# Optimization experiments

Hardware: AMD Instinct MI355X
Metric: run time of the kernel (lower is better)

The kernel has to match this reference:

```python
import jax, jax.numpy as jnp
import numpy as np

D_MODEL = 1024
NUM_HEADS = 16
LN_EPS = 1e-5


def setup_inputs() -> dict:
    key = jax.random.key(0)
    ks = jax.random.split(key, 7)
    B, S, D = 8, 1024, D_MODEL
    x = jax.random.normal(ks[0], (B, S, D), dtype=jnp.float32)
    # LayerNorm params (torch defaults: weight=1, bias=0; randomize slightly)
    ln_gamma = jnp.ones((D,), jnp.float32) + 0.02 * jax.random.normal(ks[1], (D,), jnp.float32)
    ln_beta = 0.02 * jax.random.normal(ks[2], (D,), jnp.float32)
    # nn.MultiheadAttention params: packed in_proj [3D, D], out_proj [D, D]
    scale = 1.0 / np.sqrt(D)
    in_proj_w = scale * jax.random.normal(ks[3], (3 * D, D), dtype=jnp.float32)
    in_proj_b = jnp.zeros((3 * D,), jnp.float32)
    out_proj_w = scale * jax.random.normal(ks[4], (D, D), dtype=jnp.float32)
    out_proj_b = jnp.zeros((D,), jnp.float32)
    return {
        "x": x,
        "ln_gamma": ln_gamma,
        "ln_beta": ln_beta,
        "in_proj_w": in_proj_w,
        "in_proj_b": in_proj_b,
        "out_proj_w": out_proj_w,
        "out_proj_b": out_proj_b,
    }


def reference(x, ln_gamma, ln_beta, in_proj_w, in_proj_b, out_proj_w, out_proj_b):
    B, S, D = x.shape
    H = NUM_HEADS
    Dh = D // H

    residual = x
    # LayerNorm (torch eps=1e-5)
    mu = jnp.mean(x, axis=-1, keepdims=True)
    var = jnp.mean(jnp.square(x - mu), axis=-1, keepdims=True)
    xn = (x - mu) * jax.lax.rsqrt(var + LN_EPS) * ln_gamma + ln_beta

    # Packed QKV projection: y = xn @ in_proj_w.T + in_proj_b
    qkv = jnp.einsum("bsd,ed->bse", xn, in_proj_w) + in_proj_b  # [B,S,3D]
    q, k, v = jnp.split(qkv, 3, axis=-1)

    def heads(t):  # [B,S,D] -> [B,H,S,Dh]
        return t.reshape(B, S, H, Dh).transpose(0, 2, 1, 3)

    q, k, v = heads(q), heads(k), heads(v)

    scores = jnp.einsum("bhsd,bhtd->bhst", q, k) / np.sqrt(Dh)  # [B,H,S,S]
    probs = jax.nn.softmax(scores, axis=-1)
    ctx = jnp.einsum("bhst,bhtd->bhsd", probs, v)  # [B,H,S,Dh]
    ctx = ctx.transpose(0, 2, 1, 3).reshape(B, S, D)

    attn_out = jnp.einsum("bsd,ed->bse", ctx, out_proj_w) + out_proj_b
    # (need_weights=True would also expose probs.mean over heads; math above
    #  matches the explicit non-flash path torch falls back to)
    return attn_out + residual
```

## Files before the change

### kernel.cpp

```cpp
#include <hip/hip_runtime.h>
#include <hip/hip_bf16.h>

typedef __bf16 bf16;
typedef __bf16 bf16x8 __attribute__((ext_vector_type(8)));
typedef __bf16 bf16x4 __attribute__((ext_vector_type(4)));
typedef float  f32x4  __attribute__((ext_vector_type(4)));

#define D_MODEL 1024
#define S_LEN   1024
#define NHEAD   16
#define DH      64

#define AS1 __attribute__((address_space(1)))
#define AS3 __attribute__((address_space(3)))

__global__ void cvt_kernel(const float* __restrict__ w1, bf16* __restrict__ o1, int n1,
                           const float* __restrict__ w2, bf16* __restrict__ o2, int n2) {
    int i = blockIdx.x * blockDim.x + threadIdx.x;
    const int stride = gridDim.x * blockDim.x;
    for (; i < n1 + n2; i += stride) {
        const float4 v = (i < n1) ? ((const float4*)w1)[i] : ((const float4*)w2)[i - n1];
        bf16x4 r;
        r[0] = (bf16)v.x; r[1] = (bf16)v.y; r[2] = (bf16)v.z; r[3] = (bf16)v.w;
        if (i < n1) ((bf16x4*)o1)[i] = r; else ((bf16x4*)o2)[i - n1] = r;
    }
}

__global__ __launch_bounds__(256) void ln_kernel(const float* __restrict__ x,
        const float* __restrict__ gamma, const float* __restrict__ beta,
        bf16* __restrict__ xn) {
    const int row = blockIdx.x;
    const int tid = threadIdx.x;
    const float4 v = ((const float4*)(x + (size_t)row * D_MODEL))[tid];
    float s  = v.x + v.y + v.z + v.w;
    float s2 = v.x*v.x + v.y*v.y + v.z*v.z + v.w*v.w;
    #pragma unroll
    for (int d = 1; d < 64; d <<= 1) { s += __shfl_xor(s, d); s2 += __shfl_xor(s2, d); }
    __shared__ float red[8];
    const int wave = tid >> 6;
    if ((tid & 63) == 0) { red[wave] = s; red[4 + wave] = s2; }
    __syncthreads();
    s  = red[0] + red[1] + red[2] + red[3];
    s2 = red[4] + red[5] + red[6] + red[7];
    const float mu   = s * (1.0f / D_MODEL);
    const float var  = s2 * (1.0f / D_MODEL) - mu * mu;
    const float rstd = rsqrtf(var + 1e-5f);
    const float4 g = ((const float4*)gamma)[tid];
    const float4 b = ((const float4*)beta)[tid];
    bf16x4 o;
    o[0] = (bf16)((v.x - mu) * rstd * g.x + b.x);
    o[1] = (bf16)((v.y - mu) * rstd * g.y + b.y);
    o[2] = (bf16)((v.z - mu) * rstd * g.z + b.z);
    o[3] = (bf16)((v.w - mu) * rstd * g.w + b.w);
    ((bf16x4*)(xn + (size_t)row * D_MODEL))[tid] = o;
}

#define GEMM_MAIN_LOOP(Ab, Wb, K)                                                        \
    f32x4 acc[4][4] = {};                                                                \
    for (int kt = 0; kt < (K); kt += 64) {                                               \
        _Pragma("unroll")                                                                \
        for (int i = 0; i < 4; ++i) {                                                    \
            const int L = i * 256 + tid;                                                 \
            const int r = L >> 3, blk = L & 7;                                           \
            const int src = (blk ^ (r & 7)) * 8;                                         \
            __builtin_amdgcn_global_load_lds(                                            \
                (const AS1 void*)((Ab) + (size_t)r * (K) + kt + src),                    \
                (AS3 void*)(As + L * 8), 16, 0, 0);                                      \
            __builtin_amdgcn_global_load_lds(                                            \
                (const AS1 void*)((Wb) + (size_t)r * (K) + kt + src),                    \
                (AS3 void*)(Bs + L * 8), 16, 0, 0);                                      \
        }                                                                                \
        __syncthreads();                                                                 \
        _Pragma("unroll")                                                                \
        for (int kk = 0; kk < 2; ++kk) {                                                 \
            bf16x8 af[4], bfm[4];                                                        \
            _Pragma("unroll")                                                            \
            for (int m = 0; m < 4; ++m) {                                                \
                const int R = wr * 64 + m * 16 + (lane & 15);                            \
                af[m] = *(const bf16x8*)(As + R * 64 +                                   \
                            (((kk * 4 + (lane >> 4)) ^ (R & 7)) << 3));                  \
            }                                                                            \
            _Pragma("unroll")                                                            \
            for (int n = 0; n < 4; ++n) {                                                \
                const int R = wc * 64 + n * 16 + (lane & 15);                            \
                bfm[n] = *(const bf16x8*)(Bs + R * 64 +                                  \
                            (((kk * 4 + (lane >> 4)) ^ (R & 7)) << 3));                  \
            }                                                                            \
            _Pragma("unroll")                                                            \
            for (int m = 0; m < 4; ++m)                                                  \
                _Pragma("unroll")                                                        \
                for (int n = 0; n < 4; ++n)                                              \
                    acc[m][n] = __builtin_amdgcn_mfma_f32_16x16x32_bf16(                 \
                        af[m], bfm[n], acc[m][n], 0, 0, 0);                              \
        }                                                                                \
        __syncthreads();                                                                 \
    }

#define XCD_REMAP()                                                                      \
    const int f = blockIdx.y * gridDim.x + blockIdx.x;                                   \
    const int xcd = f & 7;                                                               \
    const int rank = f >> 3;                                                             \
    const int brow = (xcd * 8 + (rank & 7)) * 128;                                       \
    const int bcol = (rank >> 3) * 128;

__global__ __launch_bounds__(256, 4) void gemm_qkv(
        const bf16* __restrict__ A, const bf16* __restrict__ W,
        const float* __restrict__ bias,
        bf16* __restrict__ q, bf16* __restrict__ k, bf16* __restrict__ vt) {
    __shared__ bf16 smem[2 * 128 * 64];
    bf16* As = smem;
    bf16* Bs = smem + 128 * 64;
    const int tid = threadIdx.x;
    const int lane = tid & 63;
    const int wave = tid >> 6;
    const int wr = wave >> 1, wc = wave & 1;
    XCD_REMAP()
    const bf16* Ab = A + (size_t)brow * 1024;
    const bf16* Wb = W + (size_t)bcol * 1024;

    GEMM_MAIN_LOOP(Ab, Wb, 1024)

    const int region = bcol >> 10;
    const int c = lane & 15, hh = lane >> 4;
    if (region == 2) {
        #pragma unroll
        for (int m = 0; m < 4; ++m) {
            #pragma unroll
            for (int n = 0; n < 4; ++n) {
                const int col = bcol + wc * 64 + n * 16 + c;
                const float bb = bias[col];
                const int e = col & 1023;
                const int h = e >> 6, dh = e & 63;
                const int row0 = brow + wr * 64 + m * 16 + hh * 4;
                const int b = row0 >> 10, s0 = row0 & 1023;
                const int bh = b * NHEAD + h;
                bf16x4 pk;
                #pragma unroll
                for (int j = 0; j < 4; ++j) pk[j] = (bf16)(acc[m][n][j] + bb);
                *(bf16x4*)(vt + ((size_t)bh * DH + dh) * S_LEN + s0) = pk;
            }
        }
    } else {
        const float qsc = (region == 0) ? 0.1803368801111244f : 1.0f;
        #pragma unroll
        for (int m = 0; m < 4; ++m) {
            #pragma unroll
            for (int n = 0; n < 4; ++n) {
                const int col = wc * 64 + n * 16 + c;
                const float bb = bias[bcol + col];
                #pragma unroll
                for (int j = 0; j < 4; ++j) {
                    const int row = wr * 64 + m * 16 + hh * 4 + j;
                    const int pb = (col >> 3) ^ (row & 7);
                    smem[row * 128 + pb * 8 + (col & 7)] = (bf16)((acc[m][n][j] + bb) * qsc);
                }
            }
        }
        __syncthreads();
        bf16* dst = (region == 0) ? q : k;
        #pragma unroll
        for (int i = 0; i < 8; ++i) {
            const int idx = i * 256 + tid;
            const int row = idx >> 4;
            const int bb = idx & 15;
            const bf16x8 vv = *(const bf16x8*)(smem + row * 128 + (bb ^ (row & 7)) * 8);
            const int grow = brow + row;
            const int s = grow & 1023, b = grow >> 10;
            const int col0 = bcol + bb * 8;
            const int e = col0 & 1023;
            const int h = e >> 6, dh = e & 63;
            *(bf16x8*)(dst + ((size_t)(b * NHEAD + h) * S_LEN + s) * DH + dh) = vv;
        }
    }
}

__global__ __launch_bounds__(256, 4) void gemm_out(
        const bf16* __restrict__ A, const bf16* __restrict__ W,
        const float* __restrict__ bias, const float* __restrict__ resid,
        float* __restrict__ out) {
    __shared__ bf16 smem[2 * 128 * 64];
    bf16* As = smem;
    bf16* Bs = smem + 128 * 64;
    const int tid = threadIdx.x;
    const int lane = tid & 63;
    const int wave = tid >> 6;
    const int wr = wave >> 1, wc = wave & 1;
    XCD_REMAP()
    const bf16* Ab = A + (size_t)brow * 1024;
    const bf16* Wb = W + (size_t)bcol * 1024;

    GEMM_MAIN_LOOP(Ab, Wb, 1024)

    #pragma unroll
    for (int m = 0; m < 4; ++m) {
        #pragma unroll
        for (int n = 0; n < 4; ++n) {
            const int col = bcol + wc * 64 + n * 16 + (lane & 15);
            const float bb = bias[col];
            #pragma unroll
            for (int j = 0; j < 4; ++j) {
                const int row = brow + wr * 64 + m * 16 + (lane >> 4) * 4 + j;
                const size_t idx = (size_t)row * D_MODEL + col;
                out[idx] = acc[m][n][j] + bb + resid[idx];
            }
        }
    }
}

__global__ __launch_bounds__(256, 3) void attn_kernel(
        const bf16* __restrict__ Q, const bf16* __restrict__ Kv,
        const bf16* __restrict__ Vt, bf16* __restrict__ ctx) {
    __shared__ bf16 KsB[2][64 * 64];
    __shared__ bf16 VsB[2][64 * 64];
    __shared__ bf16 PtB[4][32 * 64];
    const int tid = threadIdx.x;
    const int lane = tid & 63;
    const int w = tid >> 6;
    const int c = lane & 15;
    const int h = lane >> 4;
    const int bh = blockIdx.x;
    const int bb = bh >> 4, hd = bh & 15;
    const int q0 = blockIdx.y * 128 + w * 32;

    const bf16* Qh = Q + ((size_t)bh * S_LEN + q0) * DH;
    const char* Kb = (const char*)(Kv + (size_t)bh * S_LEN * DH);
    const char* Vb = (const char*)(Vt + (size_t)bh * DH * S_LEN);
    char* pw = (char*)&PtB[w][0];

    bf16x8 qf[2][2];
    #pragma unroll
    for (int nq = 0; nq < 2; ++nq)
        #pragma unroll
        for (int kk = 0; kk < 2; ++kk)
            qf[nq][kk] = *(const bf16x8*)(Qh + (16 * nq + c) * DH + kk * 32 + h * 8);

    bf16x8 ones;
    #pragma unroll
    for (int j = 0; j < 8; ++j) ones[j] = (bf16)1.0f;

    f32x4 O[2][4] = {};
    f32x4 lacc[2] = {};

#define STAGE(BB, KT) do {                                                               \
    _Pragma("unroll")                                                                    \
    for (int i = 0; i < 2; ++i) {                                                        \
        const int row = w * 16 + i * 8 + (lane >> 3);                                    \
        const int sw = ((lane & 7) ^ (row & 7)) << 4;                                    \
        const int lo = w * 2048 + i * 1024 + lane * 16;                                  \
        __builtin_amdgcn_global_load_lds(                                                \
            (const AS1 void*)(Kb + (size_t)((KT) + row) * 128 + sw),                     \
            (AS3 void*)((char*)&KsB[BB][0] + lo), 16, 0, 0);                             \
        __builtin_amdgcn_global_load_lds(                                                \
            (const AS1 void*)(Vb + (size_t)row * 2048 + (KT) * 2 + sw),                  \
            (AS3 void*)((char*)&VsB[BB][0] + lo), 16, 0, 0);                             \
    } } while (0)

    STAGE(0, 0);
    for (int t = 0; t < 16; ++t) {
        if (t < 15) {
            STAGE((t + 1) & 1, (t + 1) * 64);
            asm volatile("s_waitcnt vmcnt(4)" ::: "memory");
        } else {
            asm volatile("s_waitcnt vmcnt(0)" ::: "memory");
        }
        __builtin_amdgcn_s_barrier();
        const char* Ksb = (const char*)&KsB[t & 1][0];
        const char* Vsb = (const char*)&VsB[t & 1][0];

        f32x4 sf[2][4] = {};
        __builtin_amdgcn_s_setprio(1);
        #pragma unroll
        for (int kk = 0; kk < 2; ++kk) {
            bf16x8 kf[4];
            #pragma unroll
            for (int a = 0; a < 4; ++a)
                kf[a] = *(const bf16x8*)(Ksb + (16 * a + c) * 128 +
                                         (((4 * kk + h) ^ (c & 7)) << 4));
            #pragma unroll
            for (int nq = 0; nq < 2; ++nq)
                #pragma unroll
                for (int a = 0; a < 4; ++a)
                    sf[nq][a] = __builtin_amdgcn_mfma_f32_16x16x32_bf16(
                        kf[a], qf[nq][kk], sf[nq][a], 0, 0, 0);
        }
        __builtin_amdgcn_s_setprio(0);

        #pragma unroll
        for (int nq = 0; nq < 2; ++nq) {
            #pragma unroll
            for (int a = 0; a < 4; ++a) {
                bf16x4 pk;
                #pragma unroll
                for (int r = 0; r < 4; ++r)
                    pk[r] = (bf16)__builtin_amdgcn_exp2f(sf[nq][a][r]);
                *(bf16x4*)(pw + (16 * nq + c) * 128 +
                           (((2 * a + (h >> 1)) ^ (c & 7)) << 4) + 8 * (h & 1)) = pk;
            }
        }

        __builtin_amdgcn_s_setprio(1);
        #pragma unroll
        for (int kk = 0; kk < 2; ++kk) {
            bf16x8 pf[2], vf[4];
            #pragma unroll
            for (int mq = 0; mq < 2; ++mq)
                pf[mq] = *(const bf16x8*)(pw + (16 * mq + c) * 128 +
                                          (((4 * kk + h) ^ (c & 7)) << 4));
            #pragma unroll
            for (int f2 = 0; f2 < 4; ++f2)
                vf[f2] = *(const bf16x8*)(Vsb + (16 * f2 + c) * 128 +
                                          (((4 * kk + h) ^ (c & 7)) << 4));
            #pragma unroll
            for (int mq = 0; mq < 2; ++mq) {
                #pragma unroll
                for (int f2 = 0; f2 < 4; ++f2)
                    O[mq][f2] = __builtin_amdgcn_mfma_f32_16x16x32_bf16(
                        pf[mq], vf[f2], O[mq][f2], 0, 0, 0);
                lacc[mq] = __builtin_amdgcn_mfma_f32_16x16x32_bf16(
                    pf[mq], ones, lacc[mq], 0, 0, 0);
            }
        }
        __builtin_amdgcn_s_setprio(0);
        asm volatile("s_waitcnt lgkmcnt(0)" ::: "memory");
        __builtin_amdgcn_s_barrier();
    }
#undef STAGE

    #pragma unroll
    for (int mq = 0; mq < 2; ++mq) {
        float iv[4];
        #pragma unroll
        for (int r = 0; r < 4; ++r) iv[r] = 1.0f / lacc[mq][r];
        #pragma unroll
        for (int f2 = 0; f2 < 4; ++f2)
            #pragma unroll
            for (int r = 0; r < 4; ++r) {
                const int s = q0 + 16 * mq + 4 * h + r;
                ctx[((size_t)(bb * S_LEN + s)) * D_MODEL + hd * DH + 16 * f2 + c] =
                    (bf16)(O[mq][f2][r] * iv[r]);
            }
    }
}

extern "C" void kernel_launch(void* const* d_in, const int* in_sizes, int n_in,
                              void* d_out, int out_size, void* d_ws, size_t ws_size,
                              hipStream_t stream) {
    const float* x     = (const float*)d_in[0];
    const float* gamma = (const float*)d_in[1];
    const float* beta  = (const float*)d_in[2];
    const float* in_w  = (const float*)d_in[3];
    const float* in_b  = (const float*)d_in[4];
    const float* out_w = (const float*)d_in[5];
    const float* out_b = (const float*)d_in[6];
    float* out = (float*)d_out;

    char* ws = (char*)d_ws;
    bf16* wq  = (bf16*)(ws);
    bf16* wo  = (bf16*)(ws + 6291456);
    bf16* xn  = (bf16*)(ws + 8388608);
    bf16* q   = (bf16*)(ws + 25165824);
    bf16* kk  = (bf16*)(ws + 41943040);
    bf16* vt  = (bf16*)(ws + 58720256);
    bf16* ctx = xn;

    hipLaunchKernelGGL(cvt_kernel, dim3(512), dim3(256), 0, stream,
                       in_w, wq, 3072 * 1024 / 4, out_w, wo, 1024 * 1024 / 4);
    hipLaunchKernelGGL(ln_kernel, dim3(8192), dim3(256), 0, stream, x, gamma, beta, xn);
    hipLaunchKernelGGL(gemm_qkv, dim3(64, 24), dim3(256), 0, stream, xn, wq, in_b, q, kk, vt);
    hipLaunchKernelGGL(attn_kernel, dim3(128, 8), dim3(256), 0, stream, q, kk, vt, ctx);
    hipLaunchKernelGGL(gemm_out, dim3(64, 8), dim3(256), 0, stream, ctx, wo, out_b, x, out);
}
```

Measured before the change: 151.1 us.

## Rewrite QKV GEMM with 256x256 tiles, 8 waves and interleaved LDS pipeline

The QKV projection GEMM moves from 128x128 tiles with 4 waves to 256x256 tiles with 8 waves per block. It uses a 1D XCD-aware grid and a finer-grained schedule that interleaves global-to-LDS loads with MFMA quarter-blocks, using s_setprio and barriers. Larger tiles raise arithmetic intensity and cut global traffic per FLOP, while the interleaving aims to hide load latency. In exchange, LDS use grows to 128KB per block, the grid shrinks to 384 blocks, and the extra barriers are a risk.

```diff
diff --git a/kernel.cpp b/kernel.cpp
--- a/kernel.cpp
+++ b/kernel.cpp
@@ -103,37 +103,121 @@
     const int brow = (xcd * 8 + (rank & 7)) * 128;                                       \
     const int bcol = (rank >> 3) * 128;
 
-__global__ __launch_bounds__(256, 4) void gemm_qkv(
+__global__ __launch_bounds__(512, 2) void gemm_qkv(
         const bf16* __restrict__ A, const bf16* __restrict__ W,
         const float* __restrict__ bias,
         bf16* __restrict__ q, bf16* __restrict__ k, bf16* __restrict__ vt) {
-    __shared__ bf16 smem[2 * 128 * 64];
+    __shared__ bf16 smem[65536];
     bf16* As = smem;
-    bf16* Bs = smem + 128 * 64;
+    bf16* Bs = smem + 32768;
     const int tid = threadIdx.x;
     const int lane = tid & 63;
-    const int wave = tid >> 6;
-    const int wr = wave >> 1, wc = wave & 1;
-    XCD_REMAP()
+    const int wid = tid >> 6;
+    const int wm = wid >> 2, wn = wid & 3;
+    const int c = lane & 15, h = lane >> 4;
+    const int f = blockIdx.x;
+    const int xcd = f & 7, loc = f >> 3;
+    const int mt = xcd * 4 + (loc & 3);
+    const int nt = loc >> 2;
+    const int brow = mt * 256, bcol = nt * 256;
     const bf16* Ab = A + (size_t)brow * 1024;
     const bf16* Wb = W + (size_t)bcol * 1024;
 
-    GEMM_MAIN_LOOP(Ab, Wb, 1024)
-
-    const int region = bcol >> 10;
-    const int c = lane & 15, hh = lane >> 4;
-    if (region == 2) {
-        #pragma unroll
-        for (int m = 0; m < 4; ++m) {
+#define LOADT(XS, XG, LI, BUF, KTE) do {                                                 \
+    const int row_ = (LI) * 64 + (tid >> 3);                                             \
+    __builtin_amdgcn_global_load_lds(                                                    \
+        (const AS1 void*)((XG) + (size_t)row_ * 1024 + (KTE) +                           \
+                          (((tid & 7) ^ (row_ & 7)) << 3)),                              \
+        (AS3 void*)((XS) + (BUF) * 16384 + (LI) * 4096 + tid * 8), 16, 0, 0);            \
+} while (0)
+
+#define LDA4(BUF, MH, AF) do {                                                           \
+    _Pragma("unroll")                                                                    \
+    for (int m_ = 0; m_ < 4; ++m_) {                                                     \
+        const int R_ = wm * 128 + (MH) * 64 + m_ * 16 + c;                               \
+        _Pragma("unroll")                                                                \
+        for (int k_ = 0; k_ < 2; ++k_)                                                   \
+            AF[m_][k_] = *(const bf16x8*)(As + (BUF) * 16384 + R_ * 64 +                 \
+                           (((k_ * 4 + h) ^ (R_ & 7)) << 3));                            \
+    }                                                                                    \
+} while (0)
+
+#define LDB2(BUF, NH, BF) do {                                                           \
+    _Pragma("unroll")                                                                    \
+    for (int n_ = 0; n_ < 2; ++n_) {                                                     \
+        const int R_ = wn * 64 + (NH) * 32 + n_ * 16 + c;                                \
+        _Pragma("unroll")                                                                \
+        for (int k_ = 0; k_ < 2; ++k_)                                                   \
+            BF[n_][k_] = *(const bf16x8*)(Bs + (BUF) * 16384 + R_ * 64 +                 \
+                           (((k_ * 4 + h) ^ (R_ & 7)) << 3));                            \
+    }                                                                                    \
+} while (0)
+
+#define MFMAQ(MH, NH, AF, BF) do {                                                       \
+    __builtin_amdgcn_s_setprio(1);                                                       \
+    _Pragma("unroll")                                                                    \
+    for (int m_ = 0; m_ < 4; ++m_)                                                       \
+        _Pragma("unroll")                                                                \
+        for (int n_ = 0; n_ < 2; ++n_)                                                   \
+            _Pragma("unroll")                                                            \
+            for (int k_ = 0; k_ < 2; ++k_)                                               \
+                acc[(MH)*4 + m_][(NH)*2 + n_] =                                          \
+                    __builtin_amdgcn_mfma_f32_16x16x32_bf16(                             \
+                        AF[m_][k_], BF[n_][k_],                                          \
+                        acc[(MH)*4 + m_][(NH)*2 + n_], 0, 0, 0);                         \
+    __builtin_amdgcn_s_setprio(0);                                                       \
+} while (0)
+
+    f32x4 acc[8][4] = {};
+    #pragma unroll
+    for (int li = 0; li < 4; ++li) { LOADT(As, Ab, li, 0, 0); LOADT(Bs, Wb, li, 0, 0); }
+
+    for (int t = 0; t < 16; ++t) {
+        const int cur = t & 1, nxt = cur ^ 1;
+        const int kte = (t + 1) * 64;
+        bf16x8 af[4][2], bf0[2][2], bf1[2][2];
+        if (t < 15) {
+            LOADT(As, Ab, 0, nxt, kte); LOADT(Bs, Wb, 0, nxt, kte);
+            asm volatile("s_waitcnt vmcnt(2)" ::: "memory");
+        } else {
+            asm volatile("s_waitcnt vmcnt(0)" ::: "memory");
+        }
+        __builtin_amdgcn_s_barrier();
+        LDA4(cur, 0, af); LDB2(cur, 0, bf0);
+        MFMAQ(0, 0, af, bf0);
+        __builtin_amdgcn_s_barrier();
+        LDB2(cur, 1, bf1);
+        if (t < 15) { LOADT(As, Ab, 1, nxt, kte); LOADT(Bs, Wb, 1, nxt, kte); }
+        __builtin_amdgcn_s_barrier();
+        MFMAQ(0, 1, af, bf1);
+        __builtin_amdgcn_s_barrier();
+        LDA4(cur, 1, af);
+        if (t < 15) { LOADT(As, Ab, 2, nxt, kte); LOADT(Bs, Wb, 2, nxt, kte); }
+        __builtin_amdgcn_s_barrier();
+        MFMAQ(1, 1, af, bf1);
+        __builtin_amdgcn_s_barrier();
+        LDB2(cur, 0, bf0);
+        if (t < 15) { LOADT(As, Ab, 3, nxt, kte); LOADT(Bs, Wb, 3, nxt, kte); }
+        __builtin_amdgcn_s_barrier();
+        MFMAQ(1, 0, af, bf0);
+        __builtin_amdgcn_s_barrier();
+    }
+#undef LOADT
+#undef LDA4
+#undef LDB2
+#undef MFMAQ
+
+    if (nt >= 8) {
+        #pragma unroll
+        for (int m = 0; m < 8; ++m) {
+            const int rowg = brow + wm * 128 + m * 16 + h * 4;
+            const int b = rowg >> 10, s0 = rowg & 1023;
             #pragma unroll
             for (int n = 0; n < 4; ++n) {
-                const int col = bcol + wc * 64 + n * 16 + c;
-                const float bb = bias[col];
-                const int e = col & 1023;
-                const int h = e >> 6, dh = e & 63;
-                const int row0 = brow + wr * 64 + m * 16 + hh * 4;
-                const int b = row0 >> 10, s0 = row0 & 1023;
-                const int bh = b * NHEAD + h;
+                const int colg = bcol + wn * 64 + n * 16 + c;
+                const float bb = bias[colg];
+                const int e = colg & 1023;
+                const int bh = b * NHEAD + (e >> 6), dh = e & 63;
                 bf16x4 pk;
                 #pragma unroll
                 for (int j = 0; j < 4; ++j) pk[j] = (bf16)(acc[m][n][j] + bb);
@@ -141,35 +225,31 @@
             }
         }
     } else {
-        const float qsc = (region == 0) ? 0.1803368801111244f : 1.0f;
-        #pragma unroll
-        for (int m = 0; m < 4; ++m) {
+        const float qsc = (nt < 4) ? 0.1803368801111244f : 1.0f;
+        bf16* dst = (nt < 4) ? q : k;
+        bf16* pat = smem + wid * 8192;
+        #pragma unroll
+        for (int m = 0; m < 8; ++m)
             #pragma unroll
             for (int n = 0; n < 4; ++n) {
-                const int col = wc * 64 + n * 16 + c;
-                const float bb = bias[bcol + col];
+                const int col = n * 16 + c;
+                const float bb = bias[bcol + wn * 64 + col];
                 #pragma unroll
                 for (int j = 0; j < 4; ++j) {
-                    const int row = wr * 64 + m * 16 + hh * 4 + j;
-                    const int pb = (col >> 3) ^ (row & 7);
-                    smem[row * 128 + pb * 8 + (col & 7)] = (bf16)((acc[m][n][j] + bb) * qsc);
+                    const int rl = m * 16 + h * 4 + j;
+                    pat[rl * 64 + ((((col >> 3) ^ (rl & 7)) << 3) | (col & 7))] =
+                        (bf16)((acc[m][n][j] + bb) * qsc);
                 }
             }
-        }
-        __syncthreads();
-        bf16* dst = (region == 0) ? q : k;
-        #pragma unroll
-        for (int i = 0; i < 8; ++i) {
-            const int idx = i * 256 + tid;
-            const int row = idx >> 4;
-            const int bb = idx & 15;
-            const bf16x8 vv = *(const bf16x8*)(smem + row * 128 + (bb ^ (row & 7)) * 8);
-            const int grow = brow + row;
-            const int s = grow & 1023, b = grow >> 10;
-            const int col0 = bcol + bb * 8;
-            const int e = col0 & 1023;
-            const int h = e >> 6, dh = e & 63;
-            *(bf16x8*)(dst + ((size_t)(b * NHEAD + h) * S_LEN + s) * DH + dh) = vv;
+        const int hh8 = ((bcol + wn * 64) & 1023) >> 6;
+        #pragma unroll
+        for (int i = 0; i < 16; ++i) {
+            const int row = i * 8 + (lane >> 3);
+            const int blk = lane & 7;
+            const bf16x8 vv = *(const bf16x8*)(pat + row * 64 + ((blk ^ (row & 7)) << 3));
+            const int rowg = brow + wm * 128 + row;
+            const int b = rowg >> 10, s = rowg & 1023;
+            *(bf16x8*)(dst + ((size_t)(b * NHEAD + hh8) * S_LEN + s) * DH + blk * 8) = vv;
         }
     }
 }
@@ -366,7 +446,7 @@
     hipLaunchKernelGGL(cvt_kernel, dim3(512), dim3(256), 0, stream,
                        in_w, wq, 3072 * 1024 / 4, out_w, wo, 1024 * 1024 / 4);
     hipLaunchKernelGGL(ln_kernel, dim3(8192), dim3(256), 0, stream, x, gamma, beta, xn);
-    hipLaunchKernelGGL(gemm_qkv, dim3(64, 24), dim3(256), 0, stream, xn, wq, in_b, q, kk, vt);
+    hipLaunchKernelGGL(gemm_qkv, dim3(384), dim3(512), 0, stream, xn, wq, in_b, q, kk, vt);
     hipLaunchKernelGGL(attn_kernel, dim3(128, 8), dim3(256), 0, stream, q, kk, vt, ctx);
     hipLaunchKernelGGL(gemm_out, dim3(64, 8), dim3(256), 0, stream, ctx, wo, out_b, x, out);
 }
```

Result: slower. 157.8 us (+4.4%).
